# Optimization experiments

Hardware: AMD Instinct MI355X
Metric: run time of the kernel (lower is better)

## Reference

```python
import jax, jax.numpy as jnp
import numpy as np

N_WIRES = 8
DIM = 2 ** N_WIRES  # 256


def _rx(theta):
    # theta: [] or [N] -> [2,2] or [N,2,2] complex64
    c = jnp.cos(theta / 2)
    s = jnp.sin(theta / 2)
    return jnp.stack([jnp.stack([c + 0j, -1j * s], -1),
                      jnp.stack([-1j * s, c + 0j], -1)], -2)


def _ry(theta):
    c = jnp.cos(theta / 2)
    s = jnp.sin(theta / 2)
    return jnp.stack([jnp.stack([c + 0j, -s + 0j], -1),
                      jnp.stack([s + 0j, c + 0j], -1)], -2)


def _rz(theta):
    e = jnp.exp(-1j * theta / 2)
    z = jnp.zeros_like(e)
    return jnp.stack([jnp.stack([e, z], -1),
                      jnp.stack([z, jnp.conj(e)], -1)], -2)


def _apply_1q(state, U, wire):
    # state: [N, DIM]; U: [2,2] (shared) or [N,2,2] (per-sample)
    s = state.reshape(-1, 2 ** wire, 2, 2 ** (N_WIRES - 1 - wire))
    if U.ndim == 2:
        s = jnp.einsum('ab,nxby->nxay', U, s)
    else:
        s = jnp.einsum('nab,nxby->nxay', U, s)
    return s.reshape(-1, DIM)


def _cnot(state, c, t):
    # wire 0 = most significant bit (PennyLane convention)
    s = state.reshape((-1,) + (2,) * N_WIRES)
    ax_c = 1 + c
    s0 = jnp.take(s, 0, axis=ax_c)
    s1 = jnp.take(s, 1, axis=ax_c)
    ax_t = 1 + t if t < c else t  # target axis after control axis removed
    s1 = jnp.flip(s1, axis=ax_t)
    s = jnp.stack([s0, s1], axis=ax_c)
    return s.reshape(-1, DIM)


def _z_signs():
    idx = np.arange(DIM)
    bits = (idx[:, None] >> (N_WIRES - 1 - np.arange(N_WIRES))[None, :]) & 1
    return jnp.asarray(1.0 - 2.0 * bits, dtype=jnp.float32)  # [DIM, 8]


def _circuit(x_flat, params):
    # x_flat: [N, 8] angles; params: [8, 3]
    n = x_flat.shape[0]
    state = jnp.zeros((n, DIM), dtype=jnp.complex64).at[:, 0].set(1.0)
    for i in range(N_WIRES):
        state = _apply_1q(state, _rx(x_flat[:, i]), i)
    for i in range(N_WIRES):
        state = _apply_1q(state, _ry(params[i, 0]), i)
        state = _apply_1q(state, _rz(params[i, 1]), i)
        state = _apply_1q(state, _rx(params[i, 2]), i)
    for i in range(N_WIRES - 1):
        state = _cnot(state, i, i + 1)
    state = _cnot(state, N_WIRES - 1, 0)
    probs = state.real ** 2 + state.imag ** 2  # [N, DIM]
    return probs @ _z_signs()  # [N, 8] PauliZ expvals


def setup_inputs() -> dict:
    key = jax.random.key(0)
    ks = jax.random.split(key, 4)
    B, S = 16, 2048
    embed_dim, ffn_dim = 512, 2048
    return {
        'x': jax.random.normal(ks[0], (B, S, N_WIRES), dtype=jnp.float32),
        'params': jax.random.normal(ks[1], (N_WIRES, 3), dtype=jnp.float32),
        'W1': jax.random.normal(ks[2], (ffn_dim, N_WIRES), dtype=jnp.float32) * 0.1,
        'b1': jnp.zeros((ffn_dim,), dtype=jnp.float32),
        'W2': jax.random.normal(ks[3], (embed_dim, ffn_dim), dtype=jnp.float32) * 0.02,
        'b2': jnp.zeros((embed_dim,), dtype=jnp.float32),
    }


def reference(x, params, W1, b1, W2, b2):
    B, S, _ = x.shape
    ev = _circuit(x.reshape(-1, N_WIRES), params).reshape(B, S, N_WIRES)
    h = jax.nn.relu(ev @ W1.T + b1)
    return h @ W2.T + b2
```

## Files before the change

### kernel.cpp

```cpp
#include <hip/hip_runtime.h>
#include <hip/hip_bf16.h>

#define NS 32768
#define EMB 512
#define KDIM 2048
#define BM 128
#define BN 256
#define NITER (KDIM / 32)

typedef float f32x16 __attribute__((ext_vector_type(16)));
typedef __bf16 bf16x8 __attribute__((ext_vector_type(8)));
typedef __bf16 bf16x2 __attribute__((ext_vector_type(2)));
typedef unsigned int u32;
typedef unsigned int u32x2 __attribute__((ext_vector_type(2)));
typedef const __attribute__((address_space(1))) u32* gptr_t;
typedef __attribute__((address_space(3))) u32* lptr_t;

#if __has_builtin(__builtin_amdgcn_permlane32_swap)
#define HAS_PLS 1
#else
#define HAS_PLS 0
#endif

__device__ __forceinline__ void gload_lds16(const void* g, void* l) {
    __builtin_amdgcn_global_load_lds((gptr_t)g, (lptr_t)l, 16, 0, 0);
}

__device__ __forceinline__ u32 pkrelu(float lo, float hi) {
    union { bf16x2 h; u32 u; } c;
    c.h[0] = (__bf16)fmaxf(lo, 0.f);
    c.h[1] = (__bf16)fmaxf(hi, 0.f);
    return c.u;
}

__device__ __forceinline__ bf16x8 mk_af(u32 a, u32 b, u32 c, u32 d) {
    union { u32 u[4]; bf16x8 v; } t;
    t.u[0] = a; t.u[1] = b; t.u[2] = c; t.u[3] = d;
    return t.v;
}

__global__ __launch_bounds__(256) void k_prep(const float* __restrict__ W2,
                                              const float* __restrict__ W1,
                                              __hip_bfloat16* __restrict__ W2b,
                                              __hip_bfloat16* __restrict__ W1bg) {
    int t = threadIdx.x;
    if (blockIdx.x < 1024) {
        int i = (blockIdx.x * 256 + t) * 4;
        float4 v = *(const float4*)(W2 + i);
        __hip_bfloat16 o[4];
        o[0] = __float2bfloat16(v.x); o[1] = __float2bfloat16(v.y);
        o[2] = __float2bfloat16(v.z); o[3] = __float2bfloat16(v.w);
        *(ulong1*)(W2b + i) = *(ulong1*)o;
    } else {
        int j = (blockIdx.x - 1024) * 1024 + t * 4;
        float4 w = *(const float4*)(W1 + j);
        __hip_bfloat16 p[4];
        p[0] = __float2bfloat16(w.x); p[1] = __float2bfloat16(w.y);
        p[2] = __float2bfloat16(w.z); p[3] = __float2bfloat16(w.w);
        *(ulong1*)(W1bg + j) = *(ulong1*)p;
    }
}

__global__ __launch_bounds__(256, 2) void k_gemm(
        const float* __restrict__ x,
        const float* __restrict__ params,
        const __hip_bfloat16* __restrict__ W1bg,
        const float* __restrict__ b1,
        const __hip_bfloat16* __restrict__ W2b,
        const float* __restrict__ b2,
        float* __restrict__ C) {
    __shared__ __hip_bfloat16 Bs[2][16 * 512];
    __shared__ __hip_bfloat16 W1s[KDIM * 8];
    __shared__ float b1s[KDIM];
    __shared__ __hip_bfloat16 evs[BM * 8];

    int tid = threadIdx.x, wave = tid >> 6, lane = tid & 63;
    int l31 = lane & 31, half = lane >> 5;
    int bx = blockIdx.x, bm = bx >> 1, bn = bx & 1;

    if (tid < 128) {
        float K1[8], K2[8];
        #pragma unroll
        for (int i = 0; i < 8; i++) {
            float a = params[i*3+0], b = params[i*3+1], g = params[i*3+2];
            float sa, ca, sb, cb, sg, cg;
            __sincosf(a, &sa, &ca);
            __sincosf(b, &sb, &cb);
            __sincosf(g, &sg, &cg);
            K1[i] = sa*sb*sg + ca*cg;
            K2[i] = cb*sg;
        }
        int n = bm * BM + tid;
        float4 x0 = *(const float4*)(x + (size_t)n*8);
        float4 x1 = *(const float4*)(x + (size_t)n*8 + 4);
        float xs[8] = {x0.x, x0.y, x0.z, x0.w, x1.x, x1.y, x1.z, x1.w};
        float z[8];
        #pragma unroll
        for (int i = 0; i < 8; i++) {
            float s, c;
            __sincosf(xs[i], &s, &c);
            z[i] = c * K1[i] - s * K2[i];
        }
        float evv[8];
        float p = z[0];
        #pragma unroll
        for (int j = 1; j < 8; j++) { p *= z[j]; evv[j] = p; }
        float sfx = z[7];
        #pragma unroll
        for (int j = 6; j >= 1; j--) sfx *= z[j];
        evv[0] = sfx;
        __hip_bfloat16 o[8];
        #pragma unroll
        for (int i = 0; i < 8; i++) o[i] = __float2bfloat16(evv[i]);
        *(bf16x8*)&evs[tid * 8] = *(bf16x8*)o;
    }
    for (int i = tid; i < KDIM; i += 256) {
        *(bf16x8*)&W1s[i * 8] = *(const bf16x8*)(W1bg + (size_t)i * 8);
        b1s[i] = b1[i];
    }

    const __hip_bfloat16* gBp[4];
    #pragma unroll
    for (int i = 0; i < 4; i++) {
        int f = wave * 4 + i, ni = f >> 1, t = f & 1;
        gBp[i] = W2b + (size_t)(bn*BN + ni*32 + l31) * KDIM + t*16 + half*8;
    }
    #pragma unroll
    for (int i = 0; i < 4; i++) {
        gload_lds16(gBp[i], &Bs[0][(wave*4 + i) * 512]);
        gBp[i] += 32;
    }

    __syncthreads();

    bf16x8 evB = *(bf16x8*)&evs[(wave * 32 + l31) * 8];

    f32x16 acc[8] = {};

    for (int it = 0; it < NITER; ++it) {
        const int k0 = it * 32;
        const int cb = it & 1;

        if (it + 1 < NITER) {
            #pragma unroll
            for (int i = 0; i < 4; i++) {
                gload_lds16(gBp[i], &Bs[cb ^ 1][(wave*4 + i) * 512]);
                gBp[i] += 32;
            }
        }

        bf16x8 w1f = {};
        if (half == 0) w1f = *(const bf16x8*)&W1s[(k0 + l31) * 8];
        float4 c0 = *(const float4*)&b1s[k0 + 4*half];
        float4 c1 = *(const float4*)&b1s[k0 + 8 + 4*half];
        float4 c2 = *(const float4*)&b1s[k0 + 16 + 4*half];
        float4 c3 = *(const float4*)&b1s[k0 + 24 + 4*half];
        f32x16 h;
        h[0] = c0.x; h[1] = c0.y; h[2]  = c0.z; h[3]  = c0.w;
        h[4] = c1.x; h[5] = c1.y; h[6]  = c1.z; h[7]  = c1.w;
        h[8] = c2.x; h[9] = c2.y; h[10] = c2.z; h[11] = c2.w;
        h[12] = c3.x; h[13] = c3.y; h[14] = c3.z; h[15] = c3.w;
        h = __builtin_amdgcn_mfma_f32_32x32x16_bf16(w1f, evB, h, 0, 0, 0);

        u32 w0  = pkrelu(h[0],  h[1]);  u32 w1v = pkrelu(h[2],  h[3]);
        u32 wA  = pkrelu(h[4],  h[5]);  u32 wB  = pkrelu(h[6],  h[7]);
        u32 w2v = pkrelu(h[8],  h[9]);  u32 w3v = pkrelu(h[10], h[11]);
        u32 wC  = pkrelu(h[12], h[13]); u32 wD  = pkrelu(h[14], h[15]);
#if HAS_PLS
        { u32x2 r = __builtin_amdgcn_permlane32_swap(w0,  wA, false, false); w0  = r[0]; wA = r[1]; }
        { u32x2 r = __builtin_amdgcn_permlane32_swap(w1v, wB, false, false); w1v = r[0]; wB = r[1]; }
        { u32x2 r = __builtin_amdgcn_permlane32_swap(w2v, wC, false, false); w2v = r[0]; wC = r[1]; }
        { u32x2 r = __builtin_amdgcn_permlane32_swap(w3v, wD, false, false); w3v = r[0]; wD = r[1]; }
        bf16x8 af0 = mk_af(w0, w1v, wA, wB);
        bf16x8 af1 = mk_af(w2v, w3v, wC, wD);
#else
        int pl = lane ^ 32;
        u32 pw0 = __shfl((int)w0,  pl), pw1 = __shfl((int)w1v, pl);
        u32 pwA = __shfl((int)wA,  pl), pwB = __shfl((int)wB,  pl);
        u32 pw2 = __shfl((int)w2v, pl), pw3 = __shfl((int)w3v, pl);
        u32 pwC = __shfl((int)wC,  pl), pwD = __shfl((int)wD,  pl);
        bf16x8 af0 = half ? mk_af(pwA, pwB, wA, wB) : mk_af(w0,  w1v, pw0, pw1);
        bf16x8 af1 = half ? mk_af(pwC, pwD, wC, wD) : mk_af(w2v, w3v, pw2, pw3);
#endif

        #pragma unroll
        for (int ni = 0; ni < 8; ni++) {
            bf16x8 bfr = *(bf16x8*)&Bs[cb][(ni*2 + 0) * 512 + lane * 8];
            acc[ni] = __builtin_amdgcn_mfma_f32_32x32x16_bf16(af0, bfr, acc[ni], 0, 0, 0);
        }
        #pragma unroll
        for (int ni = 0; ni < 8; ni++) {
            bf16x8 bfr = *(bf16x8*)&Bs[cb][(ni*2 + 1) * 512 + lane * 8];
            acc[ni] = __builtin_amdgcn_mfma_f32_32x32x16_bf16(af1, bfr, acc[ni], 0, 0, 0);
        }

        __syncthreads();
    }

    int rbase = bm*BM + wave*32 + 4*half;
    #pragma unroll
    for (int ni = 0; ni < 8; ni++) {
        int col = bn*BN + ni*32 + l31;
        float bias = b2[col];
        #pragma unroll
        for (int r = 0; r < 16; r++) {
            int row = rbase + (r & 3) + 8 * (r >> 2);
            C[(size_t)row * EMB + col] = acc[ni][r] + bias;
        }
    }
}

extern "C" void kernel_launch(void* const* d_in, const int* in_sizes, int n_in,
                              void* d_out, int out_size, void* d_ws, size_t ws_size,
                              hipStream_t stream) {
    const float* x      = (const float*)d_in[0];
    const float* params = (const float*)d_in[1];
    const float* W1     = (const float*)d_in[2];
    const float* b1     = (const float*)d_in[3];
    const float* W2     = (const float*)d_in[4];
    const float* b2     = (const float*)d_in[5];
    float* out = (float*)d_out;

    char* ws = (char*)d_ws;
    __hip_bfloat16* W2b  = (__hip_bfloat16*)ws;
    __hip_bfloat16* W1bg = (__hip_bfloat16*)(ws + 2097152);

    k_prep<<<1040, 256, 0, stream>>>(W2, W1, W2b, W1bg);
    k_gemm<<<(NS/BM) * (EMB/BN), 256, 0, stream>>>(x, params, W1bg, b1, W2b, b2, out);
}
```

Measured before the change: 157.1 us.

## Reshape GEMM tile to 256x128 so each wave computes two row groups

The block tile changes from 128 rows x 256 columns to 256 rows x 128 columns. Each wave now owns 64 rows and 128 columns, so it runs two first-layer MFMAs per k-step to build two ReLU'd A-fragments and reuses each B fragment read from LDS for two accumulators. This halves the LDS B staging and global W2 traffic per block and doubles the row work, cutting B reads from LDS per MFMA. The cost is that the cheap first-layer recompute per block is duplicated across 4 column blocks instead of 2, which adds overhead.

```diff
diff --git a/kernel.cpp b/kernel.cpp
--- a/kernel.cpp
+++ b/kernel.cpp
@@ -4,8 +4,8 @@
 #define NS 32768
 #define EMB 512
 #define KDIM 2048
-#define BM 128
-#define BN 256
+#define BM 256
+#define BN 128
 #define NITER (KDIM / 32)
 
 typedef float f32x16 __attribute__((ext_vector_type(16)));
@@ -37,6 +37,30 @@
     union { u32 u[4]; bf16x8 v; } t;
     t.u[0] = a; t.u[1] = b; t.u[2] = c; t.u[3] = d;
     return t.v;
+}
+
+__device__ __forceinline__ void h_to_af(const f32x16 h, int lane, int half,
+                                        bf16x8& af0, bf16x8& af1) {
+    u32 w0  = pkrelu(h[0],  h[1]);  u32 w1v = pkrelu(h[2],  h[3]);
+    u32 wA  = pkrelu(h[4],  h[5]);  u32 wB  = pkrelu(h[6],  h[7]);
+    u32 w2v = pkrelu(h[8],  h[9]);  u32 w3v = pkrelu(h[10], h[11]);
+    u32 wC  = pkrelu(h[12], h[13]); u32 wD  = pkrelu(h[14], h[15]);
+#if HAS_PLS
+    { u32x2 r = __builtin_amdgcn_permlane32_swap(w0,  wA, false, false); w0  = r[0]; wA = r[1]; }
+    { u32x2 r = __builtin_amdgcn_permlane32_swap(w1v, wB, false, false); w1v = r[0]; wB = r[1]; }
+    { u32x2 r = __builtin_amdgcn_permlane32_swap(w2v, wC, false, false); w2v = r[0]; wC = r[1]; }
+    { u32x2 r = __builtin_amdgcn_permlane32_swap(w3v, wD, false, false); w3v = r[0]; wD = r[1]; }
+    af0 = mk_af(w0, w1v, wA, wB);
+    af1 = mk_af(w2v, w3v, wC, wD);
+#else
+    int pl = lane ^ 32;
+    u32 pw0 = __shfl((int)w0,  pl), pw1 = __shfl((int)w1v, pl);
+    u32 pwA = __shfl((int)wA,  pl), pwB = __shfl((int)wB,  pl);
+    u32 pw2 = __shfl((int)w2v, pl), pw3 = __shfl((int)w3v, pl);
+    u32 pwC = __shfl((int)wC,  pl), pwD = __shfl((int)wD,  pl);
+    af0 = half ? mk_af(pwA, pwB, wA, wB) : mk_af(w0,  w1v, pw0, pw1);
+    af1 = half ? mk_af(pwC, pwD, wC, wD) : mk_af(w2v, w3v, pw2, pw3);
+#endif
 }
 
 __global__ __launch_bounds__(256) void k_prep(const float* __restrict__ W2,
@@ -69,16 +93,16 @@
         const __hip_bfloat16* __restrict__ W2b,
         const float* __restrict__ b2,
         float* __restrict__ C) {
-    __shared__ __hip_bfloat16 Bs[2][16 * 512];
+    __shared__ __hip_bfloat16 Bs[2][8 * 512];
     __shared__ __hip_bfloat16 W1s[KDIM * 8];
     __shared__ float b1s[KDIM];
     __shared__ __hip_bfloat16 evs[BM * 8];
 
     int tid = threadIdx.x, wave = tid >> 6, lane = tid & 63;
     int l31 = lane & 31, half = lane >> 5;
-    int bx = blockIdx.x, bm = bx >> 1, bn = bx & 1;
-
-    if (tid < 128) {
+    int bx = blockIdx.x, bm = bx >> 2, bn = bx & 3;
+
+    {
         float K1[8], K2[8];
         #pragma unroll
         for (int i = 0; i < 8; i++) {
@@ -119,21 +143,22 @@
         b1s[i] = b1[i];
     }
 
-    const __hip_bfloat16* gBp[4];
+    const __hip_bfloat16* gBp[2];
     #pragma unroll
-    for (int i = 0; i < 4; i++) {
-        int f = wave * 4 + i, ni = f >> 1, t = f & 1;
+    for (int i = 0; i < 2; i++) {
+        int f = wave * 2 + i, ni = f >> 1, t = f & 1;
         gBp[i] = W2b + (size_t)(bn*BN + ni*32 + l31) * KDIM + t*16 + half*8;
     }
     #pragma unroll
-    for (int i = 0; i < 4; i++) {
-        gload_lds16(gBp[i], &Bs[0][(wave*4 + i) * 512]);
+    for (int i = 0; i < 2; i++) {
+        gload_lds16(gBp[i], &Bs[0][(wave*2 + i) * 512]);
         gBp[i] += 32;
     }
 
     __syncthreads();
 
-    bf16x8 evB = *(bf16x8*)&evs[(wave * 32 + l31) * 8];
+    bf16x8 evB0 = *(bf16x8*)&evs[(wave * 64 +      l31) * 8];
+    bf16x8 evB1 = *(bf16x8*)&evs[(wave * 64 + 32 + l31) * 8];
 
     f32x16 acc[8] = {};
 
@@ -143,8 +168,8 @@
 
         if (it + 1 < NITER) {
             #pragma unroll
-            for (int i = 0; i < 4; i++) {
-                gload_lds16(gBp[i], &Bs[cb ^ 1][(wave*4 + i) * 512]);
+            for (int i = 0; i < 2; i++) {
+                gload_lds16(gBp[i], &Bs[cb ^ 1][(wave*2 + i) * 512]);
                 gBp[i] += 32;
             }
         }
@@ -155,57 +180,47 @@
         float4 c1 = *(const float4*)&b1s[k0 + 8 + 4*half];
         float4 c2 = *(const float4*)&b1s[k0 + 16 + 4*half];
         float4 c3 = *(const float4*)&b1s[k0 + 24 + 4*half];
-        f32x16 h;
-        h[0] = c0.x; h[1] = c0.y; h[2]  = c0.z; h[3]  = c0.w;
-        h[4] = c1.x; h[5] = c1.y; h[6]  = c1.z; h[7]  = c1.w;
-        h[8] = c2.x; h[9] = c2.y; h[10] = c2.z; h[11] = c2.w;
-        h[12] = c3.x; h[13] = c3.y; h[14] = c3.z; h[15] = c3.w;
-        h = __builtin_amdgcn_mfma_f32_32x32x16_bf16(w1f, evB, h, 0, 0, 0);
-
-        u32 w0  = pkrelu(h[0],  h[1]);  u32 w1v = pkrelu(h[2],  h[3]);
-        u32 wA  = pkrelu(h[4],  h[5]);  u32 wB  = pkrelu(h[6],  h[7]);
-        u32 w2v = pkrelu(h[8],  h[9]);  u32 w3v = pkrelu(h[10], h[11]);
-        u32 wC  = pkrelu(h[12], h[13]); u32 wD  = pkrelu(h[14], h[15]);
-#if HAS_PLS
-        { u32x2 r = __builtin_amdgcn_permlane32_swap(w0,  wA, false, false); w0  = r[0]; wA = r[1]; }
-        { u32x2 r = __builtin_amdgcn_permlane32_swap(w1v, wB, false, false); w1v = r[0]; wB = r[1]; }
-        { u32x2 r = __builtin_amdgcn_permlane32_swap(w2v, wC, false, false); w2v = r[0]; wC = r[1]; }
-        { u32x2 r = __builtin_amdgcn_permlane32_swap(w3v, wD, false, false); w3v = r[0]; wD = r[1]; }
-        bf16x8 af0 = mk_af(w0, w1v, wA, wB);
-        bf16x8 af1 = mk_af(w2v, w3v, wC, wD);
-#else
-        int pl = lane ^ 32;
-        u32 pw0 = __shfl((int)w0,  pl), pw1 = __shfl((int)w1v, pl);
-        u32 pwA = __shfl((int)wA,  pl), pwB = __shfl((int)wB,  pl);
-        u32 pw2 = __shfl((int)w2v, pl), pw3 = __shfl((int)w3v, pl);
-        u32 pwC = __shfl((int)wC,  pl), pwD = __shfl((int)wD,  pl);
-        bf16x8 af0 = half ? mk_af(pwA, pwB, wA, wB) : mk_af(w0,  w1v, pw0, pw1);
-        bf16x8 af1 = half ? mk_af(pwC, pwD, wC, wD) : mk_af(w2v, w3v, pw2, pw3);
-#endif
-
-        #pragma unroll
-        for (int ni = 0; ni < 8; ni++) {
+        f32x16 hb;
+        hb[0] = c0.x; hb[1] = c0.y; hb[2]  = c0.z; hb[3]  = c0.w;
+        hb[4] = c1.x; hb[5] = c1.y; hb[6]  = c1.z; hb[7]  = c1.w;
+        hb[8] = c2.x; hb[9] = c2.y; hb[10] = c2.z; hb[11] = c2.w;
+        hb[12] = c3.x; hb[13] = c3.y; hb[14] = c3.z; hb[15] = c3.w;
+
+        f32x16 h0 = __builtin_amdgcn_mfma_f32_32x32x16_bf16(w1f, evB0, hb, 0, 0, 0);
+        bf16x8 af00, af01;
+        h_to_af(h0, lane, half, af00, af01);
+        f32x16 h1 = __builtin_amdgcn_mfma_f32_32x32x16_bf16(w1f, evB1, hb, 0, 0, 0);
+        bf16x8 af10, af11;
+        h_to_af(h1, lane, half, af10, af11);
+
+        #pragma unroll
+        for (int ni = 0; ni < 4; ni++) {
             bf16x8 bfr = *(bf16x8*)&Bs[cb][(ni*2 + 0) * 512 + lane * 8];
-            acc[ni] = __builtin_amdgcn_mfma_f32_32x32x16_bf16(af0, bfr, acc[ni], 0, 0, 0);
-        }
-        #pragma unroll
-        for (int ni = 0; ni < 8; ni++) {
+            acc[ni]     = __builtin_amdgcn_mfma_f32_32x32x16_bf16(af00, bfr, acc[ni],     0, 0, 0);
+            acc[4 + ni] = __builtin_amdgcn_mfma_f32_32x32x16_bf16(af10, bfr, acc[4 + ni], 0, 0, 0);
+        }
+        #pragma unroll
+        for (int ni = 0; ni < 4; ni++) {
             bf16x8 bfr = *(bf16x8*)&Bs[cb][(ni*2 + 1) * 512 + lane * 8];
-            acc[ni] = __builtin_amdgcn_mfma_f32_32x32x16_bf16(af1, bfr, acc[ni], 0, 0, 0);
+            acc[ni]     = __builtin_amdgcn_mfma_f32_32x32x16_bf16(af01, bfr, acc[ni],     0, 0, 0);
+            acc[4 + ni] = __builtin_amdgcn_mfma_f32_32x32x16_bf16(af11, bfr, acc[4 + ni], 0, 0, 0);
         }
 
         __syncthreads();
     }
 
-    int rbase = bm*BM + wave*32 + 4*half;
     #pragma unroll
-    for (int ni = 0; ni < 8; ni++) {
-        int col = bn*BN + ni*32 + l31;
-        float bias = b2[col];
-        #pragma unroll
-        for (int r = 0; r < 16; r++) {
-            int row = rbase + (r & 3) + 8 * (r >> 2);
-            C[(size_t)row * EMB + col] = acc[ni][r] + bias;
+    for (int rg = 0; rg < 2; rg++) {
+        int rbase = bm*BM + wave*64 + rg*32 + 4*half;
+        #pragma unroll
+        for (int ni = 0; ni < 4; ni++) {
+            int col = bn*BN + ni*32 + l31;
+            float bias = b2[col];
+            #pragma unroll
+            for (int r = 0; r < 16; r++) {
+                int row = rbase + (r & 3) + 8 * (r >> 2);
+                C[(size_t)row * EMB + col] = acc[rg*4 + ni][r] + bias;
+            }
         }
     }
 }
```

After: 151.8 us. 3.4% less time.
